# Performance work log

Measured on AMD Instinct MI355X. Metric: run time of the kernel, lower is better.

## Reference

```python
import jax, jax.numpy as jnp
import numpy as np

B = 256       # batch
H = 512       # latent_size == hidden_size == t_channels == o_channels
O_LEN = 512   # decode steps (output_shape[0])


def setup_inputs() -> dict:
    key = jax.random.key(0)
    ks = jax.random.split(key, 7)
    s = 1.0 / np.sqrt(H)
    u = lambda k, shp: jax.random.uniform(k, shp, jnp.float32, -s, s)
    return {
        "z": jax.random.normal(ks[0], (B, H), jnp.float32),
        "W_ih": u(ks[1], (4 * H, H)),   # PyTorch LSTM weight_ih_l0, gate order i,f,g,o
        "W_hh": u(ks[2], (4 * H, H)),
        "b_ih": u(ks[3], (4 * H,)),
        "b_hh": u(ks[4], (4 * H,)),
        "W_last": u(ks[5], (H, H)),     # nn.Linear(hidden_size, o_channels)
        "b_last": u(ks[6], (H,)),
    }


def reference(z, W_ih, W_hh, b_ih, b_hh, W_last, b_last):
    b = b_ih + b_hh

    def step(carry, _):
        x, h, c = carry  # each (B, H)
        gates = x @ W_ih.T + h @ W_hh.T + b  # (B, 4H)
        i, f, g, o = jnp.split(gates, 4, axis=-1)
        c = jax.nn.sigmoid(f) * c + jax.nn.sigmoid(i) * jnp.tanh(g)
        h = jax.nn.sigmoid(o) * jnp.tanh(c)
        y = h @ W_last.T + b_last  # (B, H) -> fed back as next input
        return (y, h, c), y

    # state = (z, z) as (h0, c0); first input x0 = z
    _, ys = jax.lax.scan(step, (z, z, z), None, length=O_LEN)  # ys: (O_LEN, B, H)
    return jnp.transpose(ys, (1, 0, 2))  # (B, O_LEN, H)
```

## Files before the change

### kernel.cpp

```cpp
#include <hip/hip_runtime.h>


#define HH 512
#define TT 512

typedef _Float16 half8 __attribute__((ext_vector_type(8)));
typedef float f32x4 __attribute__((ext_vector_type(4)));

__device__ __forceinline__ float sigm(float x) { return 1.0f / (1.0f + __expf(-x)); }
__device__ __forceinline__ float tanh_(float x) { return 1.0f - 2.0f / (__expf(2.0f * x) + 1.0f); }
__device__ __forceinline__ unsigned short f16b(float x) {
    _Float16 h = (_Float16)x;
    return __builtin_bit_cast(unsigned short, h);
}

__global__ __launch_bounds__(256) void k_weff(const float* __restrict__ Wih,
                                              const float* __restrict__ Whh,
                                              const float* __restrict__ Wlast,
                                              unsigned short* __restrict__ Wbig) {
    __shared__ float wih[16 * 512];
    const int tid = threadIdx.x;
    const int r0 = blockIdx.x * 16;
    for (int i = tid; i < (16 * 512) / 4; i += 256) {
        ((float4*)wih)[i] = ((const float4*)(Wih + (size_t)r0 * 512))[i];
    }
    __syncthreads();
    float acc0[16], acc1[16];
#pragma unroll
    for (int rr = 0; rr < 16; ++rr) { acc0[rr] = 0.f; acc1[rr] = 0.f; }
    const int k0 = tid * 2;
    for (int j = 0; j < 512; ++j) {
        const float2 wl = *(const float2*)(Wlast + (size_t)j * 512 + k0);
#pragma unroll
        for (int rr = 0; rr < 16; ++rr) {
            const float a = wih[rr * 512 + j];
            acc0[rr] += a * wl.x;
            acc1[rr] += a * wl.y;
        }
    }
#pragma unroll
    for (int rr = 0; rr < 16; ++rr) {
        const int gr = r0 + rr;
        const int q = gr >> 9, j = gr & 511;
        const int dst = 80 * (j >> 4) + q * 16 + (j & 15);
        const float v0 = acc0[rr] + Whh[(size_t)gr * 512 + k0];
        const float v1 = acc1[rr] + Whh[(size_t)gr * 512 + k0 + 1];
        Wbig[(size_t)dst * 512 + k0] = f16b(v0);
        Wbig[(size_t)dst * 512 + k0 + 1] = f16b(v1);
    }
}

__global__ __launch_bounds__(256) void k_pack(const float* __restrict__ z,
                                              const float* __restrict__ Wih,
                                              const float* __restrict__ Whh,
                                              const float* __restrict__ bih,
                                              const float* __restrict__ bhh,
                                              const float* __restrict__ Wlast,
                                              const float* __restrict__ blast,
                                              unsigned short* __restrict__ Wbig,
                                              unsigned short* __restrict__ W0big,
                                              float* __restrict__ biasEff,
                                              float* __restrict__ bias0,
                                              unsigned short* __restrict__ hbuf,
                                              unsigned int* __restrict__ counters) {
    const int nthr = gridDim.x * blockDim.x;
    const int gtid = blockIdx.x * blockDim.x + threadIdx.x;
    for (int e = gtid; e < 2560 * 512; e += nthr) {
        const int r = e >> 9, k = e & 511;
        const int s = r / 80, rem = r - s * 80;
        const int tau = rem >> 4, jj = rem & 15;
        const int j = s * 16 + jj;
        if (tau == 4) {
            const unsigned short v = f16b(Wlast[(size_t)j * 512 + k]);
            Wbig[e] = v;
            W0big[e] = v;
        } else {
            const int gr = tau * 512 + j;
            W0big[e] = f16b(Wih[(size_t)gr * 512 + k] + Whh[(size_t)gr * 512 + k]);
        }
    }
    for (int r = gtid; r < 2560; r += nthr) {
        const int s = r / 80, rem = r - s * 80;
        const int tau = rem >> 4, jj = rem & 15;
        const int j = s * 16 + jj;
        if (tau == 4) {
            bias0[r] = blast[j];
            biasEff[r] = blast[j];
        } else {
            const int gr = tau * 512 + j;
            const float base = bih[gr] + bhh[gr];
            float dot = 0.f;
            for (int k = 0; k < 512; ++k) dot += Wih[(size_t)gr * 512 + k] * blast[k];
            bias0[r] = base;
            biasEff[r] = base + dot;
        }
    }
    for (int e = gtid; e < 256 * 512; e += nthr) {
        const int b = e >> 9, k = e & 511;
        const int g = b >> 5, bl = b & 31;
        hbuf[((size_t)(g * 2) * 32 + bl) * 512 + k] = f16b(z[e]);
    }
    for (int e = gtid; e < 512; e += nthr) counters[e] = 0u;
}

__global__ __launch_bounds__(256, 1) void k_lstm(const unsigned short* __restrict__ Wbig,
                                                 const unsigned short* __restrict__ W0big,
                                                 const float* __restrict__ biasEff,
                                                 const float* __restrict__ bias0,
                                                 unsigned short* __restrict__ hbuf,
                                                 unsigned int* __restrict__ counters,
                                                 const float* __restrict__ z,
                                                 float* __restrict__ out) {
    const int g = blockIdx.x & 7;
    const int s = blockIdx.x >> 3;
    const int tid = threadIdx.x;
    const int wave = tid >> 6;
    const int lane = tid & 63;
    const int l15 = lane & 15;
    const int q4 = lane >> 4;

    __shared__ unsigned short hstage[32 * 520];
    __shared__ float gatesL[32 * 68];
    __shared__ float cL[32 * 18];

    const int mbase = (wave >> 1) * 16;
    const int ntile0 = (wave & 1) ? 3 : 0;
    const int ntcount = (wave & 1) ? 2 : 3;

    unsigned short* hb0 = hbuf + (size_t)(g * 2) * 32 * 512;
    unsigned short* hb1 = hb0 + 32 * 512;
    unsigned int* cnt = counters + g * 64;

    for (int idx = tid; idx < 512; idx += 256) {
        const int b = idx >> 4, jj = idx & 15;
        cL[b * 18 + jj] = z[(size_t)(g * 32 + b) * 512 + 16 * s + jj];
    }

    half8 bfrag[3][16];
#pragma unroll
    for (int tt = 0; tt < 3; ++tt) {
        if (tt < ntcount) {
            const int row = 80 * s + (ntile0 + tt) * 16 + l15;
#pragma unroll
            for (int kk = 0; kk < 16; ++kk) {
                bfrag[tt][kk] = *(const half8*)(W0big + (size_t)row * 512 + kk * 32 + q4 * 8);
            }
        }
    }
    float bias0v[3], biasEv[3];
#pragma unroll
    for (int tt = 0; tt < 3; ++tt) {
        if (tt < ntcount) {
            const int r = 80 * s + (ntile0 + tt) * 16 + l15;
            bias0v[tt] = bias0[r];
            biasEv[tt] = biasEff[r];
        } else {
            bias0v[tt] = 0.f;
            biasEv[tt] = 0.f;
        }
    }

    for (int t = 0; t <= 512; ++t) {
        {
            const unsigned short* src = (t & 1) ? hb1 : hb0;
            const char* p = (const char*)src + tid * 16;
            half8 st[8];
            asm volatile(
                "global_load_dwordx4 %0, %8, off sc0 sc1\n\t"
                "global_load_dwordx4 %1, %9, off sc0 sc1\n\t"
                "global_load_dwordx4 %2, %10, off sc0 sc1\n\t"
                "global_load_dwordx4 %3, %11, off sc0 sc1\n\t"
                "global_load_dwordx4 %4, %12, off sc0 sc1\n\t"
                "global_load_dwordx4 %5, %13, off sc0 sc1\n\t"
                "global_load_dwordx4 %6, %14, off sc0 sc1\n\t"
                "global_load_dwordx4 %7, %15, off sc0 sc1\n\t"
                "s_waitcnt vmcnt(0)"
                : "=&v"(st[0]), "=&v"(st[1]), "=&v"(st[2]), "=&v"(st[3]),
                  "=&v"(st[4]), "=&v"(st[5]), "=&v"(st[6]), "=&v"(st[7])
                : "v"(p), "v"(p + 4096), "v"(p + 8192), "v"(p + 12288),
                  "v"(p + 16384), "v"(p + 20480), "v"(p + 24576), "v"(p + 28672)
                : "memory");
#pragma unroll
            for (int i = 0; i < 8; ++i) {
                const int ci = i * 256 + tid;
                const int row = ci >> 6, col = ci & 63;
                *(half8*)(hstage + row * 520 + col * 8) = st[i];
            }
        }
        __syncthreads();

        f32x4 acc[3];
#pragma unroll
        for (int tt = 0; tt < 3; ++tt) {
            const float bv = (t == 0) ? bias0v[tt] : biasEv[tt];
            acc[tt] = (f32x4){bv, bv, bv, bv};
        }
#pragma unroll
        for (int kk = 0; kk < 16; ++kk) {
            const half8 a = *(const half8*)(hstage + (mbase + l15) * 520 + kk * 32 + q4 * 8);
#pragma unroll
            for (int tt = 0; tt < 3; ++tt) {
                if (tt < ntcount)
                    acc[tt] = __builtin_amdgcn_mfma_f32_16x16x32_f16(a, bfrag[tt][kk], acc[tt], 0, 0, 0);
            }
        }

        if ((wave & 1) && t >= 1) {
            const int n = 16 * s + l15;
#pragma unroll
            for (int r = 0; r < 4; ++r) {
                const int m = mbase + q4 * 4 + r;
                const size_t off = (size_t)(g * 32 + m) * (TT * HH) + (size_t)(t - 1) * HH + n;
                out[off] = acc[1][r];
            }
        }
        if (t == 512) break;

        {
            const int nst = (wave & 1) ? 1 : 3;
#pragma unroll
            for (int tt = 0; tt < 3; ++tt) {
                if (tt < nst) {
                    const int col = (ntile0 + tt) * 16 + l15;
#pragma unroll
                    for (int r = 0; r < 4; ++r) {
                        const int m = mbase + q4 * 4 + r;
                        gatesL[m * 68 + col] = acc[tt][r];
                    }
                }
            }
        }
        __syncthreads();

        {
            const int b = tid >> 3, jp = tid & 7;
            const int j0 = jp * 2;
            const float2 iv = *(const float2*)(gatesL + b * 68 + j0);
            const float2 fv = *(const float2*)(gatesL + b * 68 + 16 + j0);
            const float2 gv = *(const float2*)(gatesL + b * 68 + 32 + j0);
            const float2 ov = *(const float2*)(gatesL + b * 68 + 48 + j0);
            float2 cv = *(const float2*)(cL + b * 18 + j0);
            const float c0 = sigm(fv.x) * cv.x + sigm(iv.x) * tanh_(gv.x);
            const float c1 = sigm(fv.y) * cv.y + sigm(iv.y) * tanh_(gv.y);
            const float h0 = sigm(ov.x) * tanh_(c0);
            const float h1 = sigm(ov.y) * tanh_(c1);
            cv.x = c0;
            cv.y = c1;
            *(float2*)(cL + b * 18 + j0) = cv;
            unsigned short* dst = (t & 1) ? hb0 : hb1;
            const unsigned int packed = (unsigned int)f16b(h0) | ((unsigned int)f16b(h1) << 16);
            __hip_atomic_store((unsigned int*)(dst + b * 512 + 16 * s + j0), packed,
                               __ATOMIC_RELAXED, __HIP_MEMORY_SCOPE_AGENT);
        }

        if (t == 0) {
#pragma unroll
            for (int tt = 0; tt < 3; ++tt) {
                if (tt < ntcount) {
                    const int row = 80 * s + (ntile0 + tt) * 16 + l15;
#pragma unroll
                    for (int kk = 0; kk < 16; ++kk) {
                        bfrag[tt][kk] = *(const half8*)(Wbig + (size_t)row * 512 + kk * 32 + q4 * 8);
                    }
                }
            }
        }

        __syncthreads();
        if (tid == 0) {
            __hip_atomic_fetch_add(cnt, 1u, __ATOMIC_RELAXED, __HIP_MEMORY_SCOPE_AGENT);
            const unsigned int target = 32u * (unsigned)(t + 1);
            while (__hip_atomic_load(cnt, __ATOMIC_RELAXED, __HIP_MEMORY_SCOPE_AGENT) < target) {
            }
        }
        __syncthreads();
    }
}

extern "C" void kernel_launch(void* const* d_in, const int* in_sizes, int n_in,
                              void* d_out, int out_size, void* d_ws, size_t ws_size,
                              hipStream_t stream) {
    const float* z = (const float*)d_in[0];
    const float* Wih = (const float*)d_in[1];
    const float* Whh = (const float*)d_in[2];
    const float* bih = (const float*)d_in[3];
    const float* bhh = (const float*)d_in[4];
    const float* Wlast = (const float*)d_in[5];
    const float* blast = (const float*)d_in[6];
    float* out = (float*)d_out;

    char* ws = (char*)d_ws;
    unsigned short* Wbig = (unsigned short*)(ws);
    unsigned short* W0big = (unsigned short*)(ws + 2621440);
    float* biasEff = (float*)(ws + 5242880);
    float* bias0 = (float*)(ws + 5253120);
    unsigned short* hbuf = (unsigned short*)(ws + 5263360);
    unsigned int* counters = (unsigned int*)(ws + 5787648);

    k_weff<<<128, 256, 0, stream>>>(Wih, Whh, Wlast, Wbig);
    k_pack<<<512, 256, 0, stream>>>(z, Wih, Whh, bih, bhh, Wlast, blast, Wbig, W0big, biasEff,
                                    bias0, hbuf, counters);
    k_lstm<<<256, 256, 0, stream>>>(Wbig, W0big, biasEff, bias0, hbuf, counters, z, out);
}
```

Baseline: 2.251 ms.

## Replace atomic counter barrier with per-block flag array polled by all waves

Replaces the per-group atomic fetch_add counter barrier with per-block flags, each on its own 64-byte slot. Each block's thread 0 stores the step number to its flag, and every wave polls the 32 flags of its group in parallel using a ballot, which removes the second __syncthreads and atomic contention. h stores and flag accesses use inline asm with sc0 sc1 cache bypass and vmcnt waits, and output stores become nontemporal. The spin loop has a guard cap, so a long stall would silently break the barrier, and visibility ordering now depends on hand-written cache bits.

```diff
diff --git a/kernel.cpp b/kernel.cpp
--- a/kernel.cpp
+++ b/kernel.cpp
@@ -62,7 +62,7 @@
                                               float* __restrict__ biasEff,
                                               float* __restrict__ bias0,
                                               unsigned short* __restrict__ hbuf,
-                                              unsigned int* __restrict__ counters) {
+                                              unsigned int* __restrict__ flags) {
     const int nthr = gridDim.x * blockDim.x;
     const int gtid = blockIdx.x * blockDim.x + threadIdx.x;
     for (int e = gtid; e < 2560 * 512; e += nthr) {
@@ -100,7 +100,7 @@
         const int g = b >> 5, bl = b & 31;
         hbuf[((size_t)(g * 2) * 32 + bl) * 512 + k] = f16b(z[e]);
     }
-    for (int e = gtid; e < 512; e += nthr) counters[e] = 0u;
+    for (int e = gtid; e < 4096; e += nthr) flags[e] = 0u;
 }
 
 __global__ __launch_bounds__(256, 1) void k_lstm(const unsigned short* __restrict__ Wbig,
@@ -108,7 +108,7 @@
                                                  const float* __restrict__ biasEff,
                                                  const float* __restrict__ bias0,
                                                  unsigned short* __restrict__ hbuf,
-                                                 unsigned int* __restrict__ counters,
+                                                 unsigned int* __restrict__ flags,
                                                  const float* __restrict__ z,
                                                  float* __restrict__ out) {
     const int g = blockIdx.x & 7;
@@ -129,7 +129,8 @@
 
     unsigned short* hb0 = hbuf + (size_t)(g * 2) * 32 * 512;
     unsigned short* hb1 = hb0 + 32 * 512;
-    unsigned int* cnt = counters + g * 64;
+    unsigned int* smy = flags + (size_t)(g * 32 + s) * 16;
+    unsigned int* spoll = flags + (size_t)(g * 32 + (lane & 31)) * 16;
 
     for (int idx = tid; idx < 512; idx += 256) {
         const int b = idx >> 4, jj = idx & 15;
@@ -211,7 +212,7 @@
             for (int r = 0; r < 4; ++r) {
                 const int m = mbase + q4 * 4 + r;
                 const size_t off = (size_t)(g * 32 + m) * (TT * HH) + (size_t)(t - 1) * HH + n;
-                out[off] = acc[1][r];
+                __builtin_nontemporal_store(acc[1][r], &out[off]);
             }
         }
         if (t == 512) break;
@@ -236,12 +237,12 @@
             const int b = tid >> 3, jp = tid & 7;
             const int j0 = jp * 2;
             const float2 iv = *(const float2*)(gatesL + b * 68 + j0);
-            const float2 fv = *(const float2*)(gatesL + b * 68 + 16 + j0);
+            const float2 fvv = *(const float2*)(gatesL + b * 68 + 16 + j0);
             const float2 gv = *(const float2*)(gatesL + b * 68 + 32 + j0);
             const float2 ov = *(const float2*)(gatesL + b * 68 + 48 + j0);
             float2 cv = *(const float2*)(cL + b * 18 + j0);
-            const float c0 = sigm(fv.x) * cv.x + sigm(iv.x) * tanh_(gv.x);
-            const float c1 = sigm(fv.y) * cv.y + sigm(iv.y) * tanh_(gv.y);
+            const float c0 = sigm(fvv.x) * cv.x + sigm(iv.x) * tanh_(gv.x);
+            const float c1 = sigm(fvv.y) * cv.y + sigm(iv.y) * tanh_(gv.y);
             const float h0 = sigm(ov.x) * tanh_(c0);
             const float h1 = sigm(ov.y) * tanh_(c1);
             cv.x = c0;
@@ -249,8 +250,10 @@
             *(float2*)(cL + b * 18 + j0) = cv;
             unsigned short* dst = (t & 1) ? hb0 : hb1;
             const unsigned int packed = (unsigned int)f16b(h0) | ((unsigned int)f16b(h1) << 16);
-            __hip_atomic_store((unsigned int*)(dst + b * 512 + 16 * s + j0), packed,
-                               __ATOMIC_RELAXED, __HIP_MEMORY_SCOPE_AGENT);
+            unsigned int* pp = (unsigned int*)(dst + b * 512 + 16 * s + j0);
+            asm volatile("global_store_dword %0, %1, off sc0 sc1\n\ts_waitcnt vmcnt(0)" ::"v"(pp),
+                             "v"(packed)
+                         : "memory");
         }
 
         if (t == 0) {
@@ -267,13 +270,20 @@
         }
 
         __syncthreads();
+        const unsigned int tgt = (unsigned int)t + 1u;
         if (tid == 0) {
-            __hip_atomic_fetch_add(cnt, 1u, __ATOMIC_RELAXED, __HIP_MEMORY_SCOPE_AGENT);
-            const unsigned int target = 32u * (unsigned)(t + 1);
-            while (__hip_atomic_load(cnt, __ATOMIC_RELAXED, __HIP_MEMORY_SCOPE_AGENT) < target) {
-            }
-        }
-        __syncthreads();
+            asm volatile("global_store_dword %0, %1, off sc0 sc1" ::"v"(smy), "v"(tgt) : "memory");
+        }
+        {
+            unsigned int pv;
+            int guard = 0;
+            do {
+                asm volatile("global_load_dword %0, %1, off sc0 sc1\n\ts_waitcnt vmcnt(0)"
+                             : "=v"(pv)
+                             : "v"(spoll)
+                             : "memory");
+            } while (__ballot(pv >= tgt) != ~0ull && ++guard < 65536);
+        }
     }
 }
 
@@ -295,10 +305,10 @@
     float* biasEff = (float*)(ws + 5242880);
     float* bias0 = (float*)(ws + 5253120);
     unsigned short* hbuf = (unsigned short*)(ws + 5263360);
-    unsigned int* counters = (unsigned int*)(ws + 5787648);
+    unsigned int* flags = (unsigned int*)(ws + 5787648);
 
     k_weff<<<128, 256, 0, stream>>>(Wih, Whh, Wlast, Wbig);
     k_pack<<<512, 256, 0, stream>>>(z, Wih, Whh, bih, bhh, Wlast, blast, Wbig, W0big, biasEff,
-                                    bias0, hbuf, counters);
-    k_lstm<<<256, 256, 0, stream>>>(Wbig, W0big, biasEff, bias0, hbuf, counters, z, out);
-}
+                                    bias0, hbuf, flags);
+    k_lstm<<<256, 256, 0, stream>>>(Wbig, W0big, biasEff, bias0, hbuf, flags, z, out);
+}
```

New measurement: 2.880 ms. 1.28x slower.

## Halve LSTM grid so each block handles two hidden slices

Applied to the files above, without the earlier changes.

Each block now processes two 16-column hidden slices, and each wave pair covers all 32 batch rows of one slice instead of 16. This halves the number of blocks in each group's barrier from 32 to 16, which lowers contention on the spin counter and leaves fewer participants to wait on per step. In exchange, each wave issues twice as many MFMAs and each thread does twice the gate nonlinearity work per step. A spin-loop iteration guard was also added, which could let a block exit the barrier early and read stale hidden state.

```diff
diff --git a/kernel.cpp b/kernel.cpp
--- a/kernel.cpp
+++ b/kernel.cpp
@@ -112,7 +112,7 @@
                                                  const float* __restrict__ z,
                                                  float* __restrict__ out) {
     const int g = blockIdx.x & 7;
-    const int s = blockIdx.x >> 3;
+    const int pair = blockIdx.x >> 3;
     const int tid = threadIdx.x;
     const int wave = tid >> 6;
     const int lane = tid & 63;
@@ -120,10 +120,11 @@
     const int q4 = lane >> 4;
 
     __shared__ unsigned short hstage[32 * 520];
-    __shared__ float gatesL[32 * 68];
-    __shared__ float cL[32 * 18];
-
-    const int mbase = (wave >> 1) * 16;
+    __shared__ float gatesL[2 * 32 * 68];
+    __shared__ float cL[2 * 32 * 18];
+
+    const int sl = wave >> 1;
+    const int slice = 2 * pair + sl;
     const int ntile0 = (wave & 1) ? 3 : 0;
     const int ntcount = (wave & 1) ? 2 : 3;
 
@@ -131,16 +132,18 @@
     unsigned short* hb1 = hb0 + 32 * 512;
     unsigned int* cnt = counters + g * 64;
 
-    for (int idx = tid; idx < 512; idx += 256) {
-        const int b = idx >> 4, jj = idx & 15;
-        cL[b * 18 + jj] = z[(size_t)(g * 32 + b) * 512 + 16 * s + jj];
+    for (int idx = tid; idx < 1024; idx += 256) {
+        const int s2 = idx >> 9;
+        const int b = (idx >> 4) & 31, jj = idx & 15;
+        cL[(s2 * 32 + b) * 18 + jj] =
+            z[(size_t)(g * 32 + b) * 512 + 16 * (2 * pair + s2) + jj];
     }
 
     half8 bfrag[3][16];
 #pragma unroll
     for (int tt = 0; tt < 3; ++tt) {
         if (tt < ntcount) {
-            const int row = 80 * s + (ntile0 + tt) * 16 + l15;
+            const int row = 80 * slice + (ntile0 + tt) * 16 + l15;
 #pragma unroll
             for (int kk = 0; kk < 16; ++kk) {
                 bfrag[tt][kk] = *(const half8*)(W0big + (size_t)row * 512 + kk * 32 + q4 * 8);
@@ -151,7 +154,7 @@
 #pragma unroll
     for (int tt = 0; tt < 3; ++tt) {
         if (tt < ntcount) {
-            const int r = 80 * s + (ntile0 + tt) * 16 + l15;
+            const int r = 80 * slice + (ntile0 + tt) * 16 + l15;
             bias0v[tt] = bias0[r];
             biasEv[tt] = biasEff[r];
         } else {
@@ -189,29 +192,36 @@
         }
         __syncthreads();
 
-        f32x4 acc[3];
+        f32x4 acc[3][2];
 #pragma unroll
         for (int tt = 0; tt < 3; ++tt) {
             const float bv = (t == 0) ? bias0v[tt] : biasEv[tt];
-            acc[tt] = (f32x4){bv, bv, bv, bv};
+            acc[tt][0] = (f32x4){bv, bv, bv, bv};
+            acc[tt][1] = (f32x4){bv, bv, bv, bv};
         }
 #pragma unroll
         for (int kk = 0; kk < 16; ++kk) {
-            const half8 a = *(const half8*)(hstage + (mbase + l15) * 520 + kk * 32 + q4 * 8);
+            const half8 a0 = *(const half8*)(hstage + (l15)*520 + kk * 32 + q4 * 8);
+            const half8 a1 = *(const half8*)(hstage + (16 + l15) * 520 + kk * 32 + q4 * 8);
 #pragma unroll
             for (int tt = 0; tt < 3; ++tt) {
-                if (tt < ntcount)
-                    acc[tt] = __builtin_amdgcn_mfma_f32_16x16x32_f16(a, bfrag[tt][kk], acc[tt], 0, 0, 0);
+                if (tt < ntcount) {
+                    acc[tt][0] = __builtin_amdgcn_mfma_f32_16x16x32_f16(a0, bfrag[tt][kk], acc[tt][0], 0, 0, 0);
+                    acc[tt][1] = __builtin_amdgcn_mfma_f32_16x16x32_f16(a1, bfrag[tt][kk], acc[tt][1], 0, 0, 0);
+                }
             }
         }
 
         if ((wave & 1) && t >= 1) {
-            const int n = 16 * s + l15;
-#pragma unroll
-            for (int r = 0; r < 4; ++r) {
-                const int m = mbase + q4 * 4 + r;
-                const size_t off = (size_t)(g * 32 + m) * (TT * HH) + (size_t)(t - 1) * HH + n;
-                out[off] = acc[1][r];
+            const int n = 16 * slice + l15;
+#pragma unroll
+            for (int mt = 0; mt < 2; ++mt) {
+#pragma unroll
+                for (int r = 0; r < 4; ++r) {
+                    const int m = mt * 16 + q4 * 4 + r;
+                    const size_t off = (size_t)(g * 32 + m) * (TT * HH) + (size_t)(t - 1) * HH + n;
+                    out[off] = acc[1][mt][r];
+                }
             }
         }
         if (t == 512) break;
@@ -223,9 +233,12 @@
                 if (tt < nst) {
                     const int col = (ntile0 + tt) * 16 + l15;
 #pragma unroll
-                    for (int r = 0; r < 4; ++r) {
-                        const int m = mbase + q4 * 4 + r;
-                        gatesL[m * 68 + col] = acc[tt][r];
+                    for (int mt = 0; mt < 2; ++mt) {
+#pragma unroll
+                        for (int r = 0; r < 4; ++r) {
+                            const int m = mt * 16 + q4 * 4 + r;
+                            gatesL[(sl * 32 + m) * 68 + col] = acc[tt][mt][r];
+                        }
                     }
                 }
             }
@@ -235,29 +248,35 @@
         {
             const int b = tid >> 3, jp = tid & 7;
             const int j0 = jp * 2;
-            const float2 iv = *(const float2*)(gatesL + b * 68 + j0);
-            const float2 fv = *(const float2*)(gatesL + b * 68 + 16 + j0);
-            const float2 gv = *(const float2*)(gatesL + b * 68 + 32 + j0);
-            const float2 ov = *(const float2*)(gatesL + b * 68 + 48 + j0);
-            float2 cv = *(const float2*)(cL + b * 18 + j0);
-            const float c0 = sigm(fv.x) * cv.x + sigm(iv.x) * tanh_(gv.x);
-            const float c1 = sigm(fv.y) * cv.y + sigm(iv.y) * tanh_(gv.y);
-            const float h0 = sigm(ov.x) * tanh_(c0);
-            const float h1 = sigm(ov.y) * tanh_(c1);
-            cv.x = c0;
-            cv.y = c1;
-            *(float2*)(cL + b * 18 + j0) = cv;
             unsigned short* dst = (t & 1) ? hb0 : hb1;
-            const unsigned int packed = (unsigned int)f16b(h0) | ((unsigned int)f16b(h1) << 16);
-            __hip_atomic_store((unsigned int*)(dst + b * 512 + 16 * s + j0), packed,
-                               __ATOMIC_RELAXED, __HIP_MEMORY_SCOPE_AGENT);
+#pragma unroll
+            for (int s2 = 0; s2 < 2; ++s2) {
+                const float* gb = gatesL + (s2 * 32 + b) * 68;
+                const float2 iv = *(const float2*)(gb + j0);
+                const float2 fvv = *(const float2*)(gb + 16 + j0);
+                const float2 gv = *(const float2*)(gb + 32 + j0);
+                const float2 ov = *(const float2*)(gb + 48 + j0);
+                float2 cv = *(const float2*)(cL + (s2 * 32 + b) * 18 + j0);
+                const float c0 = sigm(fvv.x) * cv.x + sigm(iv.x) * tanh_(gv.x);
+                const float c1 = sigm(fvv.y) * cv.y + sigm(iv.y) * tanh_(gv.y);
+                const float h0 = sigm(ov.x) * tanh_(c0);
+                const float h1 = sigm(ov.y) * tanh_(c1);
+                cv.x = c0;
+                cv.y = c1;
+                *(float2*)(cL + (s2 * 32 + b) * 18 + j0) = cv;
+                const unsigned int packed =
+                    (unsigned int)f16b(h0) | ((unsigned int)f16b(h1) << 16);
+                __hip_atomic_store(
+                    (unsigned int*)(dst + b * 512 + 16 * (2 * pair + s2) + j0), packed,
+                    __ATOMIC_RELAXED, __HIP_MEMORY_SCOPE_AGENT);
+            }
         }
 
         if (t == 0) {
 #pragma unroll
             for (int tt = 0; tt < 3; ++tt) {
                 if (tt < ntcount) {
-                    const int row = 80 * s + (ntile0 + tt) * 16 + l15;
+                    const int row = 80 * slice + (ntile0 + tt) * 16 + l15;
 #pragma unroll
                     for (int kk = 0; kk < 16; ++kk) {
                         bfrag[tt][kk] = *(const half8*)(Wbig + (size_t)row * 512 + kk * 32 + q4 * 8);
@@ -269,8 +288,10 @@
         __syncthreads();
         if (tid == 0) {
             __hip_atomic_fetch_add(cnt, 1u, __ATOMIC_RELAXED, __HIP_MEMORY_SCOPE_AGENT);
-            const unsigned int target = 32u * (unsigned)(t + 1);
-            while (__hip_atomic_load(cnt, __ATOMIC_RELAXED, __HIP_MEMORY_SCOPE_AGENT) < target) {
+            const unsigned int target = 16u * (unsigned)(t + 1);
+            int guard = 0;
+            while (__hip_atomic_load(cnt, __ATOMIC_RELAXED, __HIP_MEMORY_SCOPE_AGENT) < target &&
+                   ++guard < 65536) {
             }
         }
         __syncthreads();
@@ -300,5 +321,5 @@
     k_weff<<<128, 256, 0, stream>>>(Wih, Whh, Wlast, Wbig);
     k_pack<<<512, 256, 0, stream>>>(z, Wih, Whh, bih, bhh, Wlast, blast, Wbig, W0big, biasEff,
                                     bias0, hbuf, counters);
-    k_lstm<<<256, 256, 0, stream>>>(Wbig, W0big, biasEff, bias0, hbuf, counters, z, out);
-}
+    k_lstm<<<128, 256, 0, stream>>>(Wbig, W0big, biasEff, bias0, hbuf, counters, z, out);
+}
```

New measurement: 2.106 ms. -6.4%, faster.

## Split batch group into two half-pipelines with per-half counters and prefetch

Applied to the files above, without the earlier changes.

The persistent LSTM kernel now runs 128 blocks, each owning two hidden slices and alternating between two 16-row batch halves per tick. While one half's h exchange and barrier are in flight, the other half's matmul and gate math proceed. The next h tile is prefetched right after polling its own counter. The per-block spin barrier is replaced by an intra-block arrival counter plus per-half global counters, both with bounded spin guards. This hides inter-block sync latency behind compute, at the cost of halving the parallel block count and doubling the number of ticks.

```diff
diff --git a/kernel.cpp b/kernel.cpp
--- a/kernel.cpp
+++ b/kernel.cpp
@@ -96,9 +96,10 @@
         }
     }
     for (int e = gtid; e < 256 * 512; e += nthr) {
-        const int b = e >> 9, k = e & 511;
-        const int g = b >> 5, bl = b & 31;
-        hbuf[((size_t)(g * 2) * 32 + bl) * 512 + k] = f16b(z[e]);
+        const int bg = e >> 9, k = e & 511;
+        const int g = bg >> 5, bl = bg & 31;
+        const int hf = bl >> 4, b16 = bl & 15;
+        hbuf[(size_t)g * 32768 + (size_t)(hf * 2) * 8192 + b16 * 512 + k] = f16b(z[e]);
     }
     for (int e = gtid; e < 512; e += nthr) counters[e] = 0u;
 }
@@ -112,35 +113,41 @@
                                                  const float* __restrict__ z,
                                                  float* __restrict__ out) {
     const int g = blockIdx.x & 7;
-    const int s = blockIdx.x >> 3;
+    const int pair = blockIdx.x >> 3;
     const int tid = threadIdx.x;
     const int wave = tid >> 6;
     const int lane = tid & 63;
     const int l15 = lane & 15;
     const int q4 = lane >> 4;
 
-    __shared__ unsigned short hstage[32 * 520];
-    __shared__ float gatesL[32 * 68];
-    __shared__ float cL[32 * 18];
-
-    const int mbase = (wave >> 1) * 16;
+    __shared__ unsigned short hstage[16 * 520];
+    __shared__ float gatesL[2 * 16 * 68];
+    __shared__ float cL[4 * 16 * 18];
+    __shared__ unsigned int arrive;
+
+    const int sl = wave >> 1;
+    const int slice = 2 * pair + sl;
     const int ntile0 = (wave & 1) ? 3 : 0;
     const int ntcount = (wave & 1) ? 2 : 3;
 
-    unsigned short* hb0 = hbuf + (size_t)(g * 2) * 32 * 512;
-    unsigned short* hb1 = hb0 + 32 * 512;
-    unsigned int* cnt = counters + g * 64;
-
-    for (int idx = tid; idx < 512; idx += 256) {
-        const int b = idx >> 4, jj = idx & 15;
-        cL[b * 18 + jj] = z[(size_t)(g * 32 + b) * 512 + 16 * s + jj];
+    unsigned short* hbg = hbuf + (size_t)g * 32768;
+    unsigned int* cntA = counters + g * 64;
+    unsigned int* cntB = counters + g * 64 + 16;
+
+    if (tid == 0) arrive = 0u;
+
+    for (int idx = tid; idx < 1024; idx += 256) {
+        const int jj = idx & 15, b = (idx >> 4) & 15;
+        const int s2 = (idx >> 8) & 1, hf = idx >> 9;
+        cL[((hf * 2 + s2) * 16 + b) * 18 + jj] =
+            z[(size_t)(g * 32 + hf * 16 + b) * 512 + 16 * (2 * pair + s2) + jj];
     }
 
     half8 bfrag[3][16];
 #pragma unroll
     for (int tt = 0; tt < 3; ++tt) {
         if (tt < ntcount) {
-            const int row = 80 * s + (ntile0 + tt) * 16 + l15;
+            const int row = 80 * slice + (ntile0 + tt) * 16 + l15;
 #pragma unroll
             for (int kk = 0; kk < 16; ++kk) {
                 bfrag[tt][kk] = *(const half8*)(W0big + (size_t)row * 512 + kk * 32 + q4 * 8);
@@ -151,7 +158,7 @@
 #pragma unroll
     for (int tt = 0; tt < 3; ++tt) {
         if (tt < ntcount) {
-            const int r = 80 * s + (ntile0 + tt) * 16 + l15;
+            const int r = 80 * slice + (ntile0 + tt) * 16 + l15;
             bias0v[tt] = bias0[r];
             biasEv[tt] = biasEff[r];
         } else {
@@ -160,44 +167,44 @@
         }
     }
 
-    for (int t = 0; t <= 512; ++t) {
-        {
-            const unsigned short* src = (t & 1) ? hb1 : hb0;
-            const char* p = (const char*)src + tid * 16;
-            half8 st[8];
-            asm volatile(
-                "global_load_dwordx4 %0, %8, off sc0 sc1\n\t"
-                "global_load_dwordx4 %1, %9, off sc0 sc1\n\t"
-                "global_load_dwordx4 %2, %10, off sc0 sc1\n\t"
-                "global_load_dwordx4 %3, %11, off sc0 sc1\n\t"
-                "global_load_dwordx4 %4, %12, off sc0 sc1\n\t"
-                "global_load_dwordx4 %5, %13, off sc0 sc1\n\t"
-                "global_load_dwordx4 %6, %14, off sc0 sc1\n\t"
-                "global_load_dwordx4 %7, %15, off sc0 sc1\n\t"
-                "s_waitcnt vmcnt(0)"
-                : "=&v"(st[0]), "=&v"(st[1]), "=&v"(st[2]), "=&v"(st[3]),
-                  "=&v"(st[4]), "=&v"(st[5]), "=&v"(st[6]), "=&v"(st[7])
-                : "v"(p), "v"(p + 4096), "v"(p + 8192), "v"(p + 12288),
-                  "v"(p + 16384), "v"(p + 20480), "v"(p + 24576), "v"(p + 28672)
-                : "memory");
-#pragma unroll
-            for (int i = 0; i < 8; ++i) {
-                const int ci = i * 256 + tid;
-                const int row = ci >> 6, col = ci & 63;
-                *(half8*)(hstage + row * 520 + col * 8) = st[i];
-            }
+    __syncthreads();
+
+    half8 st[4];
+    {
+        const char* p = (const char*)hbg + tid * 16;
+        asm volatile(
+            "global_load_dwordx4 %0, %4, off sc0 sc1\n\t"
+            "global_load_dwordx4 %1, %5, off sc0 sc1\n\t"
+            "global_load_dwordx4 %2, %6, off sc0 sc1\n\t"
+            "global_load_dwordx4 %3, %7, off sc0 sc1"
+            : "=&v"(st[0]), "=&v"(st[1]), "=&v"(st[2]), "=&v"(st[3])
+            : "v"(p), "v"(p + 4096), "v"(p + 8192), "v"(p + 12288)
+            : "memory");
+    }
+
+    for (int tick = 0; tick < 1026; ++tick) {
+        const int k = tick >> 1;
+        const int half = tick & 1;
+        const bool last = (k == 512);
+
+        asm volatile("s_waitcnt vmcnt(0)" ::: "memory");
+#pragma unroll
+        for (int i = 0; i < 4; ++i) {
+            const int ci = i * 256 + tid;
+            const int row = ci >> 6, col = ci & 63;
+            *(half8*)(hstage + row * 520 + col * 8) = st[i];
         }
         __syncthreads();
 
         f32x4 acc[3];
 #pragma unroll
         for (int tt = 0; tt < 3; ++tt) {
-            const float bv = (t == 0) ? bias0v[tt] : biasEv[tt];
+            const float bv = (k == 0) ? bias0v[tt] : biasEv[tt];
             acc[tt] = (f32x4){bv, bv, bv, bv};
         }
 #pragma unroll
         for (int kk = 0; kk < 16; ++kk) {
-            const half8 a = *(const half8*)(hstage + (mbase + l15) * 520 + kk * 32 + q4 * 8);
+            const half8 a = *(const half8*)(hstage + l15 * 520 + kk * 32 + q4 * 8);
 #pragma unroll
             for (int tt = 0; tt < 3; ++tt) {
                 if (tt < ntcount)
@@ -205,18 +212,7 @@
             }
         }
 
-        if ((wave & 1) && t >= 1) {
-            const int n = 16 * s + l15;
-#pragma unroll
-            for (int r = 0; r < 4; ++r) {
-                const int m = mbase + q4 * 4 + r;
-                const size_t off = (size_t)(g * 32 + m) * (TT * HH) + (size_t)(t - 1) * HH + n;
-                out[off] = acc[1][r];
-            }
-        }
-        if (t == 512) break;
-
-        {
+        if (!last) {
             const int nst = (wave & 1) ? 1 : 3;
 #pragma unroll
             for (int tt = 0; tt < 3; ++tt) {
@@ -224,56 +220,104 @@
                     const int col = (ntile0 + tt) * 16 + l15;
 #pragma unroll
                     for (int r = 0; r < 4; ++r) {
-                        const int m = mbase + q4 * 4 + r;
-                        gatesL[m * 68 + col] = acc[tt][r];
+                        const int m = q4 * 4 + r;
+                        gatesL[(sl * 16 + m) * 68 + col] = acc[tt][r];
                     }
                 }
             }
         }
         __syncthreads();
 
-        {
-            const int b = tid >> 3, jp = tid & 7;
+        if ((wave & 1) && k >= 1) {
+            const int n = 16 * slice + l15;
+#pragma unroll
+            for (int r = 0; r < 4; ++r) {
+                const int m = q4 * 4 + r;
+                const size_t off =
+                    (size_t)(g * 32 + half * 16 + m) * (TT * HH) + (size_t)(k - 1) * HH + n;
+                out[off] = acc[1][r];
+            }
+        }
+
+        if (!last) {
+            const int b = tid >> 4, jp = tid & 15;
             const int j0 = jp * 2;
-            const float2 iv = *(const float2*)(gatesL + b * 68 + j0);
-            const float2 fv = *(const float2*)(gatesL + b * 68 + 16 + j0);
-            const float2 gv = *(const float2*)(gatesL + b * 68 + 32 + j0);
-            const float2 ov = *(const float2*)(gatesL + b * 68 + 48 + j0);
-            float2 cv = *(const float2*)(cL + b * 18 + j0);
-            const float c0 = sigm(fv.x) * cv.x + sigm(iv.x) * tanh_(gv.x);
-            const float c1 = sigm(fv.y) * cv.y + sigm(iv.y) * tanh_(gv.y);
+            const int s2 = j0 >> 4, jj = j0 & 15;
+            const float* gb = gatesL + (s2 * 16 + b) * 68;
+            const float2 iv = *(const float2*)(gb + jj);
+            const float2 fvv = *(const float2*)(gb + 16 + jj);
+            const float2 gv = *(const float2*)(gb + 32 + jj);
+            const float2 ov = *(const float2*)(gb + 48 + jj);
+            float* cp = cL + ((half * 2 + s2) * 16 + b) * 18 + jj;
+            float2 cv = *(const float2*)cp;
+            const float c0 = sigm(fvv.x) * cv.x + sigm(iv.x) * tanh_(gv.x);
+            const float c1 = sigm(fvv.y) * cv.y + sigm(iv.y) * tanh_(gv.y);
             const float h0 = sigm(ov.x) * tanh_(c0);
             const float h1 = sigm(ov.y) * tanh_(c1);
             cv.x = c0;
             cv.y = c1;
-            *(float2*)(cL + b * 18 + j0) = cv;
-            unsigned short* dst = (t & 1) ? hb0 : hb1;
+            *(float2*)cp = cv;
+            unsigned short* hd = hbg + (half * 2 + ((k + 1) & 1)) * 8192;
             const unsigned int packed = (unsigned int)f16b(h0) | ((unsigned int)f16b(h1) << 16);
-            __hip_atomic_store((unsigned int*)(dst + b * 512 + 16 * s + j0), packed,
-                               __ATOMIC_RELAXED, __HIP_MEMORY_SCOPE_AGENT);
-        }
-
-        if (t == 0) {
-#pragma unroll
-            for (int tt = 0; tt < 3; ++tt) {
-                if (tt < ntcount) {
-                    const int row = 80 * s + (ntile0 + tt) * 16 + l15;
-#pragma unroll
-                    for (int kk = 0; kk < 16; ++kk) {
-                        bfrag[tt][kk] = *(const half8*)(Wbig + (size_t)row * 512 + kk * 32 + q4 * 8);
+            unsigned int* pp = (unsigned int*)(hd + b * 512 + 16 * (2 * pair + s2) + jj);
+            asm volatile("global_store_dword %0, %1, off sc0 sc1" ::"v"(pp), "v"(packed)
+                         : "memory");
+
+            if (tick == 1) {
+#pragma unroll
+                for (int tt = 0; tt < 3; ++tt) {
+                    if (tt < ntcount) {
+                        const int row = 80 * slice + (ntile0 + tt) * 16 + l15;
+#pragma unroll
+                        for (int kk = 0; kk < 16; ++kk) {
+                            bfrag[tt][kk] =
+                                *(const half8*)(Wbig + (size_t)row * 512 + kk * 32 + q4 * 8);
+                        }
                     }
                 }
             }
-        }
-
-        __syncthreads();
-        if (tid == 0) {
-            __hip_atomic_fetch_add(cnt, 1u, __ATOMIC_RELAXED, __HIP_MEMORY_SCOPE_AGENT);
-            const unsigned int target = 32u * (unsigned)(t + 1);
-            while (__hip_atomic_load(cnt, __ATOMIC_RELAXED, __HIP_MEMORY_SCOPE_AGENT) < target) {
-            }
-        }
-        __syncthreads();
+
+            asm volatile("s_waitcnt vmcnt(0)" ::: "memory");
+            if (lane == 0) atomicAdd(&arrive, 1u);
+            if (tid == 0) {
+                const unsigned int tgt4 = 4u * (unsigned)(tick + 1);
+                int gd = 0;
+                while (__hip_atomic_load(&arrive, __ATOMIC_RELAXED,
+                                         __HIP_MEMORY_SCOPE_WORKGROUP) < tgt4 &&
+                       ++gd < (1 << 20)) {
+                }
+                asm volatile("" ::: "memory");
+                __hip_atomic_fetch_add(half ? cntB : cntA, 1u, __ATOMIC_RELAXED,
+                                       __HIP_MEMORY_SCOPE_AGENT);
+            }
+        }
+
+        if (tick < 1025) {
+            const int nhalf = half ^ 1;
+            const int nk = half ? (k + 1) : k;
+            if (nk > 0) {
+                unsigned int* cy = nhalf ? cntB : cntA;
+                const unsigned int tgt = 16u * (unsigned)nk;
+                unsigned int pv;
+                int gd = 0;
+                do {
+                    asm volatile("global_load_dword %0, %1, off sc0 sc1\n\ts_waitcnt vmcnt(0)"
+                                 : "=v"(pv)
+                                 : "v"(cy)
+                                 : "memory");
+                } while (pv < tgt && ++gd < (1 << 17));
+            }
+            const char* p =
+                (const char*)(hbg + (nhalf * 2 + (nk & 1)) * 8192) + tid * 16;
+            asm volatile(
+                "global_load_dwordx4 %0, %4, off sc0 sc1\n\t"
+                "global_load_dwordx4 %1, %5, off sc0 sc1\n\t"
+                "global_load_dwordx4 %2, %6, off sc0 sc1\n\t"
+                "global_load_dwordx4 %3, %7, off sc0 sc1"
+                : "=&v"(st[0]), "=&v"(st[1]), "=&v"(st[2]), "=&v"(st[3])
+                : "v"(p), "v"(p + 4096), "v"(p + 8192), "v"(p + 12288)
+                : "memory");
+        }
     }
 }
 
@@ -300,5 +344,5 @@
     k_weff<<<128, 256, 0, stream>>>(Wih, Whh, Wlast, Wbig);
     k_pack<<<512, 256, 0, stream>>>(z, Wih, Whh, bih, bhh, Wlast, blast, Wbig, W0big, biasEff,
                                     bias0, hbuf, counters);
-    k_lstm<<<256, 256, 0, stream>>>(Wbig, W0big, biasEff, bias0, hbuf, counters, z, out);
-}
+    k_lstm<<<128, 256, 0, stream>>>(Wbig, W0big, biasEff, bias0, hbuf, counters, z, out);
+}
```

Result: slower. 4.186 ms (+86.0%).
